# Optimization experiments

Hardware: AMD Instinct MI355X
Metric: run time of the kernel (lower is better)

The kernel has to match this reference:

```python
import jax, jax.numpy as jnp
import numpy as np

ALPHA = 0.2          # LeakyReLU negative slope
NEG_INF = -9e15      # masking value from the original module


def setup_inputs() -> dict:
    key = jax.random.key(0)
    kw, ka, k1, k2, k3 = jax.random.split(key, 5)
    B, N1, N2, F, O = 4, 2048, 2048, 256, 256
    word = jax.random.normal(kw, (B, N2, F), dtype=jnp.float32)
    # 0/1 hypergraph incidence matrix (float, as in the torch module)
    adj = jax.random.randint(ka, (B, N1, N2), 0, 2).astype(jnp.float32)
    stdv = 1.0 / np.sqrt(O)
    W1 = jax.random.uniform(k1, (F, O), jnp.float32, -stdv, stdv)
    W2 = jax.random.uniform(k2, (F, O), jnp.float32, -stdv, stdv)
    w3 = jax.random.uniform(k3, (2 * O, 1), jnp.float32, -stdv, stdv)
    return {"word": word, "adj": adj, "W1": W1, "W2": W2, "w3": w3}


def reference(word, adj, W1, W2, w3):
    # word: [B, N2, F]; adj: [B, N1, N2]; W1/W2: [F, O]; w3: [2O, 1]
    O = W1.shape[1]
    # mean-pool neighbor features per hyperedge (row-normalized adj)
    deg = jnp.sum(adj, axis=-1, keepdims=True)                 # [B, N1, 1]
    deg = jnp.where(deg > 0, deg, jnp.ones_like(deg))
    mp = jnp.matmul(adj / deg, word)                           # [B, N1, F]
    # The original builds 4D tensors h1[b,i,j,:] = adj[b,i,j]*word[b,j,:] and
    # h_mp[b,i,j,:] = adj[b,i,j]*mp[b,i,:], projects both and dots with w3.
    # Since scaling commutes with the linear maps, the scalar score is
    #   adj[b,i,j] * (word[b,j] @ W1 @ w3_a + mp[b,i] @ W2 @ w3_b)
    w3a = w3[:O, 0]                                            # pairs with w1h
    w3b = w3[O:, 0]                                            # pairs with w2h
    s1 = jnp.einsum('bnf,fo,o->bn', word, W1, w3a)             # [B, N2]
    s2 = jnp.einsum('bnf,fo,o->bn', mp, W2, w3b)               # [B, N1]
    pre = adj * (s2[:, :, None] + s1[:, None, :])              # [B, N1, N2]
    alpha = jnp.exp(jax.nn.leaky_relu(pre, ALPHA))
    attention = jnp.where(adj > 0, alpha, NEG_INF)
    attention_edge = jax.nn.softmax(attention, axis=2)         # over N2
    edge = jnp.matmul(attention_edge, word)                    # [B, N1, F]
    return edge
```

## Files before the change

kernel.cpp:

```cpp
#include <hip/hip_runtime.h>

#define B 4
#define N 2048
#define F 256
#define O 256
#define LOG2E 1.4426950408889634f
#define NEG_BIG -9000000000000000.0f

typedef _Float16 f16;
typedef f16 f16x4 __attribute__((ext_vector_type(4)));
typedef f16 f16x8 __attribute__((ext_vector_type(8)));
typedef float f32x16 __attribute__((ext_vector_type(16)));

#define WS_V1 0
#define WS_V2 256
#define WS_T1 512
#define WS_T2 (512 + B*N)
#define WT_OFF (1u << 20)
#define WGT_OFF (8u << 20)

__device__ __forceinline__ float alpha_of(float pre2) {
  return __builtin_amdgcn_exp2f(fmaxf(pre2, 0.2f * pre2));
}

__global__ __launch_bounds__(256) void k_v(const float* __restrict__ W1,
                                           const float* __restrict__ W2,
                                           const float* __restrict__ w3,
                                           float* __restrict__ ws) {
  int tid = threadIdx.x;
  int lane = tid & 63;
  int f = blockIdx.x * 4 + (tid >> 6);
  float a = 0.f, b = 0.f;
  #pragma unroll
  for (int k = 0; k < 4; ++k) {
    int o = lane + 64 * k;
    a += W1[f * O + o] * w3[o];
    b += W2[f * O + o] * w3[O + o];
  }
  #pragma unroll
  for (int off = 32; off > 0; off >>= 1) {
    a += __shfl_down(a, off);
    b += __shfl_down(b, off);
  }
  if (lane == 0) {
    ws[WS_V1 + f] = a;
    ws[WS_V2 + f] = b;
  }
}

__global__ __launch_bounds__(256) void k_prep(const float* __restrict__ word,
                                              float* __restrict__ ws,
                                              f16* __restrict__ wordT) {
  __shared__ float v1s[F], v2s[F];
  __shared__ __align__(16) f16 tile[F][40];
  int t = threadIdx.x;
  int k0 = blockIdx.x * 32;
  int b = blockIdx.y;

  if (t < 64)       ((float4*)v1s)[t]      = ((const float4*)(ws + WS_V1))[t];
  else if (t < 128) ((float4*)v2s)[t - 64] = ((const float4*)(ws + WS_V2))[t - 64];
  __syncthreads();

  int r = t >> 3;
  int cg = t & 7;
  const float* wrow = word + ((size_t)(b * N + k0 + r)) * F;
  float a = 0.f, bb = 0.f;
  #pragma unroll
  for (int i = 0; i < 8; ++i) {
    int c = i * 32 + cg * 4;
    float4 w = *(const float4*)(wrow + c);
    float4 x1 = *(const float4*)(v1s + c);
    float4 x2 = *(const float4*)(v2s + c);
    a  += w.x * x1.x + w.y * x1.y + w.z * x1.z + w.w * x1.w;
    bb += w.x * x2.x + w.y * x2.y + w.z * x2.z + w.w * x2.w;
    tile[c + 0][r] = (f16)w.x;
    tile[c + 1][r] = (f16)w.y;
    tile[c + 2][r] = (f16)w.z;
    tile[c + 3][r] = (f16)w.w;
  }
  #pragma unroll
  for (int off = 4; off > 0; off >>= 1) {
    a  += __shfl_down(a, off);
    bb += __shfl_down(bb, off);
  }
  if (cg == 0) {
    ws[WS_T1 + b * N + k0 + r] = a * LOG2E;
    ws[WS_T2 + b * N + k0 + r] = bb;
  }
  __syncthreads();

  size_t base = (size_t)b * F * N;
  #pragma unroll
  for (int i = 0; i < 4; ++i) {
    int idx = t + 256 * i;
    int ft = idx >> 7, c = (idx >> 6) & 1, l = idx & 63;
    int f = ft * 32 + (l & 31);
    int rr = c * 16 + ((l >> 5) * 8);
    f16x8 h = *(const f16x8*)&tile[f][rr];
    *(f16x8*)(wordT + base + ((size_t)((ft * 128 + (k0 >> 4) + c) * 64 + l)) * 8) = h;
  }
}

__global__ __launch_bounds__(512) void k_weights(const float* __restrict__ adj,
                                                 const float* __restrict__ ws,
                                                 f16* __restrict__ Wt) {
  __shared__ __align__(16) f16 tile[8][2056];
  int t = threadIdx.x;
  int wid = t >> 6, l = t & 63;
  int a = blockIdx.x;
  int row = a * 8 + wid;
  int b = row >> 11;
  const float* arow = adj + (size_t)row * N;
  const float* t1b = ws + WS_T1 + b * N;
  const float* t2b = ws + WS_T2 + b * N;

  float deg = 0.f, dot = 0.f;
  unsigned mb = 0u;
  #pragma unroll
  for (int i = 0; i < 8; ++i) {
    int k = i * 256 + l * 4;
    float4 av = *(const float4*)(arow + k);
    float4 uv = *(const float4*)(t2b + k);
    deg += av.x + av.y + av.z + av.w;
    dot += av.x * uv.x + av.y * uv.y + av.z * uv.z + av.w * uv.w;
    mb |= (av.x > 0.f ? (1u << (4 * i))     : 0u) |
          (av.y > 0.f ? (1u << (4 * i + 1)) : 0u) |
          (av.z > 0.f ? (1u << (4 * i + 2)) : 0u) |
          (av.w > 0.f ? (1u << (4 * i + 3)) : 0u);
  }
  #pragma unroll
  for (int off = 32; off > 0; off >>= 1) {
    deg += __shfl_xor(deg, off);
    dot += __shfl_xor(dot, off);
  }
  float degc = deg > 0.f ? deg : 1.f;
  float s2p = (dot / degc) * LOG2E;

  float al[32];
  float m = NEG_BIG;
  #pragma unroll
  for (int i = 0; i < 8; ++i) {
    int k = i * 256 + l * 4;
    float4 pv = *(const float4*)(t1b + k);
    float p0 = pv.x + s2p, p1 = pv.y + s2p, p2 = pv.z + s2p, p3 = pv.w + s2p;
    al[4 * i + 0] = ((mb >> (4 * i + 0)) & 1u) ? alpha_of(p0) : NEG_BIG;
    al[4 * i + 1] = ((mb >> (4 * i + 1)) & 1u) ? alpha_of(p1) : NEG_BIG;
    al[4 * i + 2] = ((mb >> (4 * i + 2)) & 1u) ? alpha_of(p2) : NEG_BIG;
    al[4 * i + 3] = ((mb >> (4 * i + 3)) & 1u) ? alpha_of(p3) : NEG_BIG;
    m = fmaxf(m, fmaxf(fmaxf(al[4 * i], al[4 * i + 1]), fmaxf(al[4 * i + 2], al[4 * i + 3])));
  }
  #pragma unroll
  for (int off = 32; off > 0; off >>= 1) m = fmaxf(m, __shfl_xor(m, off));

  float negmL = -m * LOG2E;
  float z = 0.f;
  #pragma unroll
  for (int j = 0; j < 32; ++j) {
    float e = __builtin_amdgcn_exp2f(fmaf(al[j], LOG2E, negmL));
    z += e;
    al[j] = e;
  }
  #pragma unroll
  for (int off = 32; off > 0; off >>= 1) z += __shfl_xor(z, off);
  float sc, wn;
  if (deg > 0.f) { sc = 1.0f / z; wn = 0.f; }
  else           { sc = 0.f;      wn = 1.0f / (float)N; }

  #pragma unroll
  for (int i = 0; i < 8; ++i) {
    f16x4 h;
    #pragma unroll
    for (int c = 0; c < 4; ++c) {
      int j = 4 * i + c;
      float w = ((mb >> j) & 1u) ? al[j] * sc : wn;
      h[c] = (f16)w;
    }
    *(f16x4*)&tile[wid][i * 256 + l * 4] = h;
  }
  __syncthreads();

  size_t base16 = (size_t)(a >> 2) * (128 * 64) + 8 * (a & 3);
  #pragma unroll
  for (int s = 0; s < 4; ++s) {
    int u = s * 512 + t;
    int r8 = u & 7, half = (u >> 3) & 1, kc = u >> 4;
    f16x8 v = *(const f16x8*)&tile[r8][kc * 16 + half * 8];
    *(f16x8*)(Wt + (base16 + (size_t)kc * 64 + half * 32 + r8) * 8) = v;
  }
}

__global__ __launch_bounds__(512) void k_gemm(const f16* __restrict__ Wt,
                                              const f16* __restrict__ wordT,
                                              float* __restrict__ out) {
  int bid = blockIdx.x;
  int sbid = (bid & 7) * 32 + (bid >> 3);
  int rb2 = sbid >> 1, fh = sbid & 1;
  int t = threadIdx.x;
  int wid = t >> 6, l = t & 63;
  int r32 = rb2 * 2 + (wid >> 2);
  int ftile = fh * 4 + (wid & 3);
  int b = r32 >> 6;

  const f16* ap = Wt + (size_t)r32 * (128 * 512) + l * 8;
  const f16* bp = wordT + (size_t)b * (F * N) + (size_t)ftile * (128 * 512) + l * 8;

  f32x16 acc = {0.f,0.f,0.f,0.f,0.f,0.f,0.f,0.f,0.f,0.f,0.f,0.f,0.f,0.f,0.f,0.f};
  #pragma unroll 8
  for (int c = 0; c < 128; ++c) {
    f16x8 af = *(const f16x8*)(ap + (size_t)c * 512);
    f16x8 bf = *(const f16x8*)(bp + (size_t)c * 512);
    acc = __builtin_amdgcn_mfma_f32_32x32x16_f16(af, bf, acc, 0, 0, 0);
  }

  int row0 = r32 * 32;
  int fcol = ftile * 32 + (l & 31);
  #pragma unroll
  for (int reg = 0; reg < 16; ++reg) {
    int lr = (reg & 3) + 8 * (reg >> 2) + 4 * (l >> 5);
    out[(size_t)(row0 + lr) * F + fcol] = acc[reg];
  }
}

extern "C" void kernel_launch(void* const* d_in, const int* in_sizes, int n_in,
                              void* d_out, int out_size, void* d_ws, size_t ws_size,
                              hipStream_t stream) {
  const float* word = (const float*)d_in[0];
  const float* adj  = (const float*)d_in[1];
  const float* W1   = (const float*)d_in[2];
  const float* W2   = (const float*)d_in[3];
  const float* w3   = (const float*)d_in[4];
  float* out = (float*)d_out;
  float* ws  = (float*)d_ws;
  f16* wordT = (f16*)((char*)d_ws + WT_OFF);
  f16* Wt    = (f16*)((char*)d_ws + WGT_OFF);

  k_v<<<64, 256, 0, stream>>>(W1, W2, w3, ws);
  k_prep<<<dim3(N / 32, B), 256, 0, stream>>>(word, ws, wordT);
  k_weights<<<(B * N) / 8, 512, 0, stream>>>(adj, ws, Wt);
  k_gemm<<<256, 512, 0, stream>>>(Wt, wordT, out);
}
```

Baseline: 143.7 us.

## Fuse softmax weight computation with the GEMM using LDS-resident attention tiles

Merges the attention-weight kernel and the MFMA GEMM into one kernel. Each 512-thread block computes masked-softmax weights for 32 adjacency rows, stores them as fp16 in a 128KB XOR-swizzled LDS tile, then runs the 32x32x16 MFMA loop reading A from LDS and B from global wordT. This removes the global write and re-read of the fp16 weight matrix and one kernel launch. In exchange it needs 144KB of dynamic LDS, which limits each CU to one block, so there is less latency hiding while streaming adj. Each block also now reads all eight feature tiles of wordT.

Result: faster. 131.8 us (-8.2%).

```diff
diff --git a/kernel.cpp b/kernel.cpp
--- a/kernel.cpp
+++ b/kernel.cpp
@@ -8,7 +8,6 @@
 #define NEG_BIG -9000000000000000.0f
 
 typedef _Float16 f16;
-typedef f16 f16x4 __attribute__((ext_vector_type(4)));
 typedef f16 f16x8 __attribute__((ext_vector_type(8)));
 typedef float f32x16 __attribute__((ext_vector_type(16)));
 
@@ -17,7 +16,6 @@
 #define WS_T1 512
 #define WS_T2 (512 + B*N)
 #define WT_OFF (1u << 20)
-#define WGT_OFF (8u << 20)
 
 __device__ __forceinline__ float alpha_of(float pre2) {
   return __builtin_amdgcn_exp2f(fmaxf(pre2, 0.2f * pre2));
@@ -101,119 +99,123 @@
   }
 }
 
-__global__ __launch_bounds__(512) void k_weights(const float* __restrict__ adj,
-                                                 const float* __restrict__ ws,
-                                                 f16* __restrict__ Wt) {
-  __shared__ __align__(16) f16 tile[8][2056];
-  int t = threadIdx.x;
-  int wid = t >> 6, l = t & 63;
-  int a = blockIdx.x;
-  int row = a * 8 + wid;
-  int b = row >> 11;
-  const float* arow = adj + (size_t)row * N;
-  const float* t1b = ws + WS_T1 + b * N;
-  const float* t2b = ws + WS_T2 + b * N;
-
-  float deg = 0.f, dot = 0.f;
-  unsigned mb = 0u;
-  #pragma unroll
-  for (int i = 0; i < 8; ++i) {
-    int k = i * 256 + l * 4;
-    float4 av = *(const float4*)(arow + k);
-    float4 uv = *(const float4*)(t2b + k);
-    deg += av.x + av.y + av.z + av.w;
-    dot += av.x * uv.x + av.y * uv.y + av.z * uv.z + av.w * uv.w;
-    mb |= (av.x > 0.f ? (1u << (4 * i))     : 0u) |
-          (av.y > 0.f ? (1u << (4 * i + 1)) : 0u) |
-          (av.z > 0.f ? (1u << (4 * i + 2)) : 0u) |
-          (av.w > 0.f ? (1u << (4 * i + 3)) : 0u);
-  }
-  #pragma unroll
-  for (int off = 32; off > 0; off >>= 1) {
-    deg += __shfl_xor(deg, off);
-    dot += __shfl_xor(dot, off);
-  }
-  float degc = deg > 0.f ? deg : 1.f;
-  float s2p = (dot / degc) * LOG2E;
-
-  float al[32];
-  float m = NEG_BIG;
-  #pragma unroll
-  for (int i = 0; i < 8; ++i) {
-    int k = i * 256 + l * 4;
-    float4 pv = *(const float4*)(t1b + k);
-    float p0 = pv.x + s2p, p1 = pv.y + s2p, p2 = pv.z + s2p, p3 = pv.w + s2p;
-    al[4 * i + 0] = ((mb >> (4 * i + 0)) & 1u) ? alpha_of(p0) : NEG_BIG;
-    al[4 * i + 1] = ((mb >> (4 * i + 1)) & 1u) ? alpha_of(p1) : NEG_BIG;
-    al[4 * i + 2] = ((mb >> (4 * i + 2)) & 1u) ? alpha_of(p2) : NEG_BIG;
-    al[4 * i + 3] = ((mb >> (4 * i + 3)) & 1u) ? alpha_of(p3) : NEG_BIG;
-    m = fmaxf(m, fmaxf(fmaxf(al[4 * i], al[4 * i + 1]), fmaxf(al[4 * i + 2], al[4 * i + 3])));
-  }
-  #pragma unroll
-  for (int off = 32; off > 0; off >>= 1) m = fmaxf(m, __shfl_xor(m, off));
-
-  float negmL = -m * LOG2E;
-  float z = 0.f;
-  #pragma unroll
-  for (int j = 0; j < 32; ++j) {
-    float e = __builtin_amdgcn_exp2f(fmaf(al[j], LOG2E, negmL));
-    z += e;
-    al[j] = e;
-  }
-  #pragma unroll
-  for (int off = 32; off > 0; off >>= 1) z += __shfl_xor(z, off);
-  float sc, wn;
-  if (deg > 0.f) { sc = 1.0f / z; wn = 0.f; }
-  else           { sc = 0.f;      wn = 1.0f / (float)N; }
-
-  #pragma unroll
-  for (int i = 0; i < 8; ++i) {
-    f16x4 h;
-    #pragma unroll
-    for (int c = 0; c < 4; ++c) {
-      int j = 4 * i + c;
-      float w = ((mb >> j) & 1u) ? al[j] * sc : wn;
-      h[c] = (f16)w;
-    }
-    *(f16x4*)&tile[wid][i * 256 + l * 4] = h;
-  }
-  __syncthreads();
-
-  size_t base16 = (size_t)(a >> 2) * (128 * 64) + 8 * (a & 3);
-  #pragma unroll
-  for (int s = 0; s < 4; ++s) {
-    int u = s * 512 + t;
-    int r8 = u & 7, half = (u >> 3) & 1, kc = u >> 4;
-    f16x8 v = *(const f16x8*)&tile[r8][kc * 16 + half * 8];
-    *(f16x8*)(Wt + (base16 + (size_t)kc * 64 + half * 32 + r8) * 8) = v;
-  }
-}
-
-__global__ __launch_bounds__(512) void k_gemm(const f16* __restrict__ Wt,
-                                              const f16* __restrict__ wordT,
-                                              float* __restrict__ out) {
-  int bid = blockIdx.x;
-  int sbid = (bid & 7) * 32 + (bid >> 3);
-  int rb2 = sbid >> 1, fh = sbid & 1;
-  int t = threadIdx.x;
-  int wid = t >> 6, l = t & 63;
-  int r32 = rb2 * 2 + (wid >> 2);
-  int ftile = fh * 4 + (wid & 3);
-  int b = r32 >> 6;
-
-  const f16* ap = Wt + (size_t)r32 * (128 * 512) + l * 8;
-  const f16* bp = wordT + (size_t)b * (F * N) + (size_t)ftile * (128 * 512) + l * 8;
+__global__ __launch_bounds__(512, 2) void k_sg(const float* __restrict__ adj,
+                                               const float* __restrict__ ws,
+                                               const f16* __restrict__ wordT,
+                                               float* __restrict__ out) {
+  extern __shared__ __align__(16) char smem[];
+  float* t1S = (float*)(smem + 131072);
+  float* t2S = (float*)(smem + 131072 + 8192);
+
+  const int t = threadIdx.x;
+  const int wv = t >> 6, l = t & 63;
+  const int row0 = blockIdx.x * 32;
+  const int b = row0 >> 11;
+
+  {
+    float4 v0 = *(const float4*)(ws + WS_T1 + b * N + t * 4);
+    float4 v1 = *(const float4*)(ws + WS_T2 + b * N + t * 4);
+    *(float4*)(t1S + t * 4) = v0;
+    *(float4*)(t2S + t * 4) = v1;
+  }
+  __syncthreads();
+
+  #pragma unroll 1
+  for (int rr = 0; rr < 4; ++rr) {
+    const int lrow = wv * 4 + rr;
+    const float* arow = adj + (size_t)(row0 + lrow) * N;
+
+    float deg = 0.f, dot = 0.f;
+    unsigned mb = 0u;
+    #pragma unroll
+    for (int i = 0; i < 4; ++i) {
+      int k = i * 512 + l * 8;
+      float4 a0 = *(const float4*)(arow + k);
+      float4 a1 = *(const float4*)(arow + k + 4);
+      float4 u0 = *(const float4*)(t2S + k);
+      float4 u1 = *(const float4*)(t2S + k + 4);
+      deg += a0.x + a0.y + a0.z + a0.w + a1.x + a1.y + a1.z + a1.w;
+      dot += a0.x * u0.x + a0.y * u0.y + a0.z * u0.z + a0.w * u0.w +
+             a1.x * u1.x + a1.y * u1.y + a1.z * u1.z + a1.w * u1.w;
+      mb |= (a0.x > 0.f ? (1u << (8 * i + 0)) : 0u) |
+            (a0.y > 0.f ? (1u << (8 * i + 1)) : 0u) |
+            (a0.z > 0.f ? (1u << (8 * i + 2)) : 0u) |
+            (a0.w > 0.f ? (1u << (8 * i + 3)) : 0u) |
+            (a1.x > 0.f ? (1u << (8 * i + 4)) : 0u) |
+            (a1.y > 0.f ? (1u << (8 * i + 5)) : 0u) |
+            (a1.z > 0.f ? (1u << (8 * i + 6)) : 0u) |
+            (a1.w > 0.f ? (1u << (8 * i + 7)) : 0u);
+    }
+    #pragma unroll
+    for (int off = 32; off > 0; off >>= 1) {
+      deg += __shfl_xor(deg, off);
+      dot += __shfl_xor(dot, off);
+    }
+    float degc = deg > 0.f ? deg : 1.f;
+    float s2p = (dot / degc) * LOG2E;
+
+    float al[32];
+    float m = NEG_BIG;
+    #pragma unroll
+    for (int i = 0; i < 4; ++i) {
+      int k = i * 512 + l * 8;
+      float4 p0 = *(const float4*)(t1S + k);
+      float4 p1 = *(const float4*)(t1S + k + 4);
+      const float pv[8] = {p0.x, p0.y, p0.z, p0.w, p1.x, p1.y, p1.z, p1.w};
+      #pragma unroll
+      for (int c = 0; c < 8; ++c) {
+        int j = 8 * i + c;
+        al[j] = ((mb >> j) & 1u) ? alpha_of(pv[c] + s2p) : NEG_BIG;
+        m = fmaxf(m, al[j]);
+      }
+    }
+    #pragma unroll
+    for (int off = 32; off > 0; off >>= 1) m = fmaxf(m, __shfl_xor(m, off));
+
+    float negmL = -m * LOG2E;
+    float z = 0.f;
+    #pragma unroll
+    for (int j = 0; j < 32; ++j) {
+      float e = __builtin_amdgcn_exp2f(fmaf(al[j], LOG2E, negmL));
+      z += e;
+      al[j] = e;
+    }
+    #pragma unroll
+    for (int off = 32; off > 0; off >>= 1) z += __shfl_xor(z, off);
+    float sc, wn;
+    if (deg > 0.f) { sc = 1.0f / z; wn = 0.f; }
+    else           { sc = 0.f;      wn = 1.0f / (float)N; }
+
+    #pragma unroll
+    for (int i = 0; i < 4; ++i) {
+      f16x8 h;
+      #pragma unroll
+      for (int c = 0; c < 8; ++c) {
+        int j = 8 * i + c;
+        float w = ((mb >> j) & 1u) ? al[j] * sc : wn;
+        h[c] = (f16)w;
+      }
+      unsigned byteoff = (unsigned)(lrow * 4096 + i * 1024 + l * 16) ^ ((unsigned)(lrow & 7) << 4);
+      *(f16x8*)(smem + byteoff) = h;
+    }
+  }
+  __syncthreads();
+
+  const int ftile = wv;
+  const int rowl = l & 31;
+  const unsigned rbase = (unsigned)(rowl * 4096 + (l >> 5) * 16);
+  const unsigned rx = (unsigned)(rowl & 7) << 4;
+  const f16* bp = wordT + (size_t)b * (F * N) + (size_t)ftile * (128 * 512) + (size_t)l * 8;
 
   f32x16 acc = {0.f,0.f,0.f,0.f,0.f,0.f,0.f,0.f,0.f,0.f,0.f,0.f,0.f,0.f,0.f,0.f};
   #pragma unroll 8
-  for (int c = 0; c < 128; ++c) {
-    f16x8 af = *(const f16x8*)(ap + (size_t)c * 512);
-    f16x8 bf = *(const f16x8*)(bp + (size_t)c * 512);
+  for (int kc = 0; kc < 128; ++kc) {
+    f16x8 af = *(const f16x8*)(smem + ((rbase + kc * 32) ^ rx));
+    f16x8 bf = *(const f16x8*)(bp + (size_t)kc * 512);
     acc = __builtin_amdgcn_mfma_f32_32x32x16_f16(af, bf, acc, 0, 0, 0);
   }
 
-  int row0 = r32 * 32;
-  int fcol = ftile * 32 + (l & 31);
+  const int fcol = ftile * 32 + (l & 31);
   #pragma unroll
   for (int reg = 0; reg < 16; ++reg) {
     int lr = (reg & 3) + 8 * (reg >> 2) + 4 * (l >> 5);
@@ -232,10 +234,14 @@
   float* out = (float*)d_out;
   float* ws  = (float*)d_ws;
   f16* wordT = (f16*)((char*)d_ws + WT_OFF);
-  f16* Wt    = (f16*)((char*)d_ws + WGT_OFF);
+
+  static bool s_attr = false;
+  if (!s_attr) {
+    hipFuncSetAttribute((const void*)k_sg, hipFuncAttributeMaxDynamicSharedMemorySize, 147456);
+    s_attr = true;
+  }
 
   k_v<<<64, 256, 0, stream>>>(W1, W2, w3, ws);
   k_prep<<<dim3(N / 32, B), 256, 0, stream>>>(word, ws, wordT);
-  k_weights<<<(B * N) / 8, 512, 0, stream>>>(adj, ws, Wt);
-  k_gemm<<<256, 512, 0, stream>>>(Wt, wordT, out);
-}
+  k_sg<<<(B * N) / 32, 512, 147456, stream>>>(adj, ws, wordT, out);
+}
```

## Fuse softmax weight computation with GEMM, keeping weights in shared memory

Applied to the files above, without the earlier changes.

Merges the attention-weight kernel and the GEMM kernel into one kernel. Each block computes fp16 softmax weights for 16 rows into swizzled LDS, then runs 16x16x32 MFMAs against a re-laid-out wordT. This removes the global write and re-read of the 32 MB fp16 weight matrix and one kernel launch. In exchange each block re-reads all of wordT for its batch with smaller 16-row tiles, and uses 80 KB of dynamic LDS per block, which limits occupancy.

Measured after the change: 131.9 us. 1.09x faster.

```diff
diff --git a/kernel.cpp b/kernel.cpp
--- a/kernel.cpp
+++ b/kernel.cpp
@@ -10,14 +10,13 @@
 typedef _Float16 f16;
 typedef f16 f16x4 __attribute__((ext_vector_type(4)));
 typedef f16 f16x8 __attribute__((ext_vector_type(8)));
-typedef float f32x16 __attribute__((ext_vector_type(16)));
+typedef float f32x4 __attribute__((ext_vector_type(4)));
 
 #define WS_V1 0
 #define WS_V2 256
 #define WS_T1 512
 #define WS_T2 (512 + B*N)
 #define WT_OFF (1u << 20)
-#define WGT_OFF (8u << 20)
 
 __device__ __forceinline__ float alpha_of(float pre2) {
   return __builtin_amdgcn_exp2f(fmaxf(pre2, 0.2f * pre2));
@@ -90,134 +89,131 @@
   __syncthreads();
 
   size_t base = (size_t)b * F * N;
-  #pragma unroll
-  for (int i = 0; i < 4; ++i) {
-    int idx = t + 256 * i;
-    int ft = idx >> 7, c = (idx >> 6) & 1, l = idx & 63;
-    int f = ft * 32 + (l & 31);
-    int rr = c * 16 + ((l >> 5) * 8);
-    f16x8 h = *(const f16x8*)&tile[f][rr];
-    *(f16x8*)(wordT + base + ((size_t)((ft * 128 + (k0 >> 4) + c) * 64 + l)) * 8) = h;
-  }
-}
-
-__global__ __launch_bounds__(512) void k_weights(const float* __restrict__ adj,
-                                                 const float* __restrict__ ws,
-                                                 f16* __restrict__ Wt) {
-  __shared__ __align__(16) f16 tile[8][2056];
-  int t = threadIdx.x;
-  int wid = t >> 6, l = t & 63;
-  int a = blockIdx.x;
-  int row = a * 8 + wid;
-  int b = row >> 11;
-  const float* arow = adj + (size_t)row * N;
-  const float* t1b = ws + WS_T1 + b * N;
-  const float* t2b = ws + WS_T2 + b * N;
-
-  float deg = 0.f, dot = 0.f;
-  unsigned mb = 0u;
-  #pragma unroll
-  for (int i = 0; i < 8; ++i) {
-    int k = i * 256 + l * 4;
-    float4 av = *(const float4*)(arow + k);
-    float4 uv = *(const float4*)(t2b + k);
-    deg += av.x + av.y + av.z + av.w;
-    dot += av.x * uv.x + av.y * uv.y + av.z * uv.z + av.w * uv.w;
-    mb |= (av.x > 0.f ? (1u << (4 * i))     : 0u) |
-          (av.y > 0.f ? (1u << (4 * i + 1)) : 0u) |
-          (av.z > 0.f ? (1u << (4 * i + 2)) : 0u) |
-          (av.w > 0.f ? (1u << (4 * i + 3)) : 0u);
-  }
-  #pragma unroll
-  for (int off = 32; off > 0; off >>= 1) {
-    deg += __shfl_xor(deg, off);
-    dot += __shfl_xor(dot, off);
-  }
-  float degc = deg > 0.f ? deg : 1.f;
-  float s2p = (dot / degc) * LOG2E;
-
-  float al[32];
-  float m = NEG_BIG;
-  #pragma unroll
-  for (int i = 0; i < 8; ++i) {
-    int k = i * 256 + l * 4;
-    float4 pv = *(const float4*)(t1b + k);
-    float p0 = pv.x + s2p, p1 = pv.y + s2p, p2 = pv.z + s2p, p3 = pv.w + s2p;
-    al[4 * i + 0] = ((mb >> (4 * i + 0)) & 1u) ? alpha_of(p0) : NEG_BIG;
-    al[4 * i + 1] = ((mb >> (4 * i + 1)) & 1u) ? alpha_of(p1) : NEG_BIG;
-    al[4 * i + 2] = ((mb >> (4 * i + 2)) & 1u) ? alpha_of(p2) : NEG_BIG;
-    al[4 * i + 3] = ((mb >> (4 * i + 3)) & 1u) ? alpha_of(p3) : NEG_BIG;
-    m = fmaxf(m, fmaxf(fmaxf(al[4 * i], al[4 * i + 1]), fmaxf(al[4 * i + 2], al[4 * i + 3])));
-  }
-  #pragma unroll
-  for (int off = 32; off > 0; off >>= 1) m = fmaxf(m, __shfl_xor(m, off));
-
-  float negmL = -m * LOG2E;
-  float z = 0.f;
-  #pragma unroll
-  for (int j = 0; j < 32; ++j) {
-    float e = __builtin_amdgcn_exp2f(fmaf(al[j], LOG2E, negmL));
-    z += e;
-    al[j] = e;
-  }
-  #pragma unroll
-  for (int off = 32; off > 0; off >>= 1) z += __shfl_xor(z, off);
-  float sc, wn;
-  if (deg > 0.f) { sc = 1.0f / z; wn = 0.f; }
-  else           { sc = 0.f;      wn = 1.0f / (float)N; }
-
-  #pragma unroll
-  for (int i = 0; i < 8; ++i) {
-    f16x4 h;
-    #pragma unroll
-    for (int c = 0; c < 4; ++c) {
-      int j = 4 * i + c;
-      float w = ((mb >> j) & 1u) ? al[j] * sc : wn;
-      h[c] = (f16)w;
-    }
-    *(f16x4*)&tile[wid][i * 256 + l * 4] = h;
-  }
-  __syncthreads();
-
-  size_t base16 = (size_t)(a >> 2) * (128 * 64) + 8 * (a & 3);
+  int kc = k0 >> 5;
   #pragma unroll
   for (int s = 0; s < 4; ++s) {
-    int u = s * 512 + t;
-    int r8 = u & 7, half = (u >> 3) & 1, kc = u >> 4;
-    f16x8 v = *(const f16x8*)&tile[r8][kc * 16 + half * 8];
-    *(f16x8*)(Wt + (base16 + (size_t)kc * 64 + half * 32 + r8) * 8) = v;
-  }
-}
-
-__global__ __launch_bounds__(512) void k_gemm(const f16* __restrict__ Wt,
-                                              const f16* __restrict__ wordT,
-                                              float* __restrict__ out) {
-  int bid = blockIdx.x;
-  int sbid = (bid & 7) * 32 + (bid >> 3);
-  int rb2 = sbid >> 1, fh = sbid & 1;
-  int t = threadIdx.x;
-  int wid = t >> 6, l = t & 63;
-  int r32 = rb2 * 2 + (wid >> 2);
-  int ftile = fh * 4 + (wid & 3);
-  int b = r32 >> 6;
-
-  const f16* ap = Wt + (size_t)r32 * (128 * 512) + l * 8;
-  const f16* bp = wordT + (size_t)b * (F * N) + (size_t)ftile * (128 * 512) + l * 8;
-
-  f32x16 acc = {0.f,0.f,0.f,0.f,0.f,0.f,0.f,0.f,0.f,0.f,0.f,0.f,0.f,0.f,0.f,0.f};
+    int u = t + 256 * s;
+    int ft = u >> 6, l2 = u & 63;
+    f16x8 h = *(const f16x8*)&tile[ft * 16 + (l2 & 15)][(l2 >> 4) * 8];
+    *(f16x8*)(wordT + base + ((size_t)(ft * 64 + kc) * 64 + l2) * 8) = h;
+  }
+}
+
+__global__ __launch_bounds__(512, 4) void k_sg(const float* __restrict__ adj,
+                                               const float* __restrict__ ws,
+                                               const f16* __restrict__ wordT,
+                                               float* __restrict__ out) {
+  extern __shared__ __align__(16) char smem[];
+  float* t1S = (float*)(smem + 65536);
+  float* t2S = (float*)(smem + 73728);
+
+  const int t = threadIdx.x;
+  const int wv = t >> 6, l = t & 63;
+  const int bid = blockIdx.x;
+  const int sbid = (bid & 7) * 64 + (bid >> 3);
+  const int row0 = sbid * 16;
+  const int b = row0 >> 11;
+
+  *(float4*)(t1S + t * 4) = *(const float4*)(ws + WS_T1 + b * N + t * 4);
+  *(float4*)(t2S + t * 4) = *(const float4*)(ws + WS_T2 + b * N + t * 4);
+  __syncthreads();
+
+  #pragma unroll 1
+  for (int rr = 0; rr < 2; ++rr) {
+    const int lrow = wv * 2 + rr;
+    const float* arow = adj + (size_t)(row0 + lrow) * N;
+
+    float deg = 0.f, dot = 0.f;
+    unsigned mb = 0u;
+    #pragma unroll
+    for (int i = 0; i < 8; ++i) {
+      int k = i * 256 + l * 4;
+      float4 av = *(const float4*)(arow + k);
+      float4 uv = *(const float4*)(t2S + k);
+      deg += av.x + av.y + av.z + av.w;
+      dot += av.x * uv.x + av.y * uv.y + av.z * uv.z + av.w * uv.w;
+      mb |= (av.x > 0.f ? (1u << (4 * i + 0)) : 0u) |
+            (av.y > 0.f ? (1u << (4 * i + 1)) : 0u) |
+            (av.z > 0.f ? (1u << (4 * i + 2)) : 0u) |
+            (av.w > 0.f ? (1u << (4 * i + 3)) : 0u);
+    }
+    #pragma unroll
+    for (int off = 32; off > 0; off >>= 1) {
+      deg += __shfl_xor(deg, off);
+      dot += __shfl_xor(dot, off);
+    }
+    float degc = deg > 0.f ? deg : 1.f;
+    float s2p = (dot / degc) * LOG2E;
+
+    float al[32];
+    float m = NEG_BIG;
+    #pragma unroll
+    for (int i = 0; i < 8; ++i) {
+      int k = i * 256 + l * 4;
+      float4 pv = *(const float4*)(t1S + k);
+      const float p[4] = {pv.x, pv.y, pv.z, pv.w};
+      #pragma unroll
+      for (int c = 0; c < 4; ++c) {
+        int j = 4 * i + c;
+        al[j] = ((mb >> j) & 1u) ? alpha_of(p[c] + s2p) : NEG_BIG;
+        m = fmaxf(m, al[j]);
+      }
+    }
+    #pragma unroll
+    for (int off = 32; off > 0; off >>= 1) m = fmaxf(m, __shfl_xor(m, off));
+
+    float negmL = -m * LOG2E;
+    float z = 0.f;
+    #pragma unroll
+    for (int j = 0; j < 32; ++j) {
+      float e = __builtin_amdgcn_exp2f(fmaf(al[j], LOG2E, negmL));
+      z += e;
+      al[j] = e;
+    }
+    #pragma unroll
+    for (int off = 32; off > 0; off >>= 1) z += __shfl_xor(z, off);
+    float sc, wn;
+    if (deg > 0.f) { sc = 1.0f / z; wn = 0.f; }
+    else           { sc = 0.f;      wn = 1.0f / (float)N; }
+
+    #pragma unroll
+    for (int i = 0; i < 8; ++i) {
+      f16x4 h;
+      #pragma unroll
+      for (int c = 0; c < 4; ++c) {
+        int j = 4 * i + c;
+        float w = ((mb >> j) & 1u) ? al[j] * sc : wn;
+        h[c] = (f16)w;
+      }
+      unsigned byteoff = (unsigned)(lrow * 4096 + i * 512 + l * 8) ^ ((unsigned)(lrow & 7) << 4);
+      *(f16x4*)(smem + byteoff) = h;
+    }
+  }
+  __syncthreads();
+
+  const int ft0 = wv * 2;
+  const unsigned abase = (unsigned)((l & 15) * 4096 + (l >> 4) * 16);
+  const unsigned ax = ((unsigned)(l & 7)) << 4;
+  const f16* bp0 = wordT + (size_t)b * (F * N) + ((size_t)ft0 * 64 * 64 + (size_t)l) * 8;
+  const f16* bp1 = bp0 + (size_t)64 * 512;
+
+  f32x4 acc0 = {0.f, 0.f, 0.f, 0.f};
+  f32x4 acc1 = {0.f, 0.f, 0.f, 0.f};
   #pragma unroll 8
-  for (int c = 0; c < 128; ++c) {
-    f16x8 af = *(const f16x8*)(ap + (size_t)c * 512);
-    f16x8 bf = *(const f16x8*)(bp + (size_t)c * 512);
-    acc = __builtin_amdgcn_mfma_f32_32x32x16_f16(af, bf, acc, 0, 0, 0);
-  }
-
-  int row0 = r32 * 32;
-  int fcol = ftile * 32 + (l & 31);
-  #pragma unroll
-  for (int reg = 0; reg < 16; ++reg) {
-    int lr = (reg & 3) + 8 * (reg >> 2) + 4 * (l >> 5);
-    out[(size_t)(row0 + lr) * F + fcol] = acc[reg];
+  for (int kc = 0; kc < 64; ++kc) {
+    f16x8 af = *(const f16x8*)(smem + ((abase + kc * 64) ^ ax));
+    f16x8 bf0 = *(const f16x8*)(bp0 + (size_t)kc * 512);
+    f16x8 bf1 = *(const f16x8*)(bp1 + (size_t)kc * 512);
+    acc0 = __builtin_amdgcn_mfma_f32_16x16x32_f16(af, bf0, acc0, 0, 0, 0);
+    acc1 = __builtin_amdgcn_mfma_f32_16x16x32_f16(af, bf1, acc1, 0, 0, 0);
+  }
+
+  const int orow = row0 + (l >> 4) * 4;
+  const int c0 = ft0 * 16 + (l & 15);
+  #pragma unroll
+  for (int reg = 0; reg < 4; ++reg) {
+    out[(size_t)(orow + reg) * F + c0]      = acc0[reg];
+    out[(size_t)(orow + reg) * F + c0 + 16] = acc1[reg];
   }
 }
 
@@ -232,10 +228,14 @@
   float* out = (float*)d_out;
   float* ws  = (float*)d_ws;
   f16* wordT = (f16*)((char*)d_ws + WT_OFF);
-  f16* Wt    = (f16*)((char*)d_ws + WGT_OFF);
+
+  static bool s_attr = false;
+  if (!s_attr) {
+    hipFuncSetAttribute((const void*)k_sg, hipFuncAttributeMaxDynamicSharedMemorySize, 81920);
+    s_attr = true;
+  }
 
   k_v<<<64, 256, 0, stream>>>(W1, W2, w3, ws);
   k_prep<<<dim3(N / 32, B), 256, 0, stream>>>(word, ws, wordT);
-  k_weights<<<(B * N) / 8, 512, 0, stream>>>(adj, ws, Wt);
-  k_gemm<<<256, 512, 0, stream>>>(Wt, wordT, out);
-}
+  k_sg<<<(B * N) / 16, 512, 81920, stream>>>(adj, ws, wordT, out);
+}
```
